# Performance work log

Hardware: AMD Instinct MI355X
Metric: run time of the kernel (lower is better)

Reference implementation:

```python
import jax, jax.numpy as jnp
import numpy as np

ATTEN = 32  # window half-size; window = 2*ATTEN + 1


def _pos_enc(seq_len, hidden_size):
    # Faithful to original: pos_enc[pos, j] = pos / 10000**(2*(j//2)/hidden_size)
    # then sin on even columns, cos on odd columns. Shape [seq_len, seq_len].
    pos = jnp.arange(seq_len, dtype=jnp.float32)[:, None]
    j = jnp.arange(seq_len)
    inv = jnp.power(jnp.float32(10000.0), (2.0 * (j // 2).astype(jnp.float32)) / hidden_size)
    angle = pos / inv[None, :]
    return jnp.where((j % 2 == 0)[None, :], jnp.sin(angle), jnp.cos(angle))


def setup_inputs() -> dict:
    key = jax.random.key(0)
    ks = jax.random.split(key, 8)
    B, S, D_in, H, D_out = 4, 2048, 2048, 128, 2
    sd_in = 1.0 / np.sqrt(D_in)
    sd_h = 1.0 / np.sqrt(H)
    return {
        "x": jax.random.normal(ks[0], (B, S, D_in), dtype=jnp.float32),
        "W1": jax.random.normal(ks[1], (D_in, H), dtype=jnp.float32) * sd_in,
        "b1": jnp.zeros((H,), dtype=jnp.float32),
        "Wq": jax.random.normal(ks[2], (H, H), dtype=jnp.float32) * sd_h,
        "Wk": jax.random.normal(ks[3], (H, H), dtype=jnp.float32) * sd_h,
        "Wv": jax.random.normal(ks[4], (H, H), dtype=jnp.float32) * sd_h,
        "Wo": jax.random.normal(ks[5], (H, D_out), dtype=jnp.float32) * sd_h,
        "bo": jnp.zeros((D_out,), dtype=jnp.float32),
    }


def reference(x, W1, b1, Wq, Wk, Wv, Wo, bo):
    B, S, _ = x.shape
    H = W1.shape[1]
    scale = jnp.float32(np.sqrt(float(H)))

    x = x + _pos_enc(S, H)[None]                      # [B,S,D_in] (D_in == S)
    h = jax.nn.relu(x @ W1 + b1)                      # [B,S,H]

    # Replicate pad + roll(+wraparound) + stack + slice via a gather.
    # x_nei[b,i,j] = padded[b, (i + 2a - j) mod (S+2a)], j in [0, 2a].
    a = ATTEN
    L = S + 2 * a
    padded = jnp.pad(h, ((0, 0), (a, a), (0, 0)))     # [B,L,H]
    idx = (jnp.arange(S)[:, None] + 2 * a - jnp.arange(2 * a + 1)[None, :]) % L
    x_nei = padded[:, idx, :]                         # [B,S,2a+1,H]

    q = h @ Wq                                        # [B,S,H]
    k = x_nei @ Wk                                    # [B,S,2a+1,H]
    v = x_nei @ Wv                                    # [B,S,2a+1,H]

    scores = jnp.einsum('bid,bijd->bij', q, k) / scale
    atten_weights = jax.nn.softmax(scores, axis=-1)   # [B,S,2a+1]
    context = jnp.einsum('bij,bijd->bid', atten_weights, v) / scale  # extra /sqrt(H), faithful to source
    output = context @ Wo + bo                        # [B,S,D_out]
    return output, atten_weights
```

## Files before the change

kernel.cpp:

```cpp
#include <hip/hip_runtime.h>
#include <hip/hip_bf16.h>

typedef __attribute__((ext_vector_type(8))) _Float16 half8;
typedef __attribute__((ext_vector_type(4))) _Float16 half4;
typedef __attribute__((ext_vector_type(4))) float f32x4;

#define MFMAH(a,b,c) __builtin_amdgcn_mfma_f32_16x16x32_f16(a,b,c,0,0,0)

__device__ __forceinline__ float posenc(float sf, int k) {
  float c = exp2f((float)(k >> 1) * -0.2076205059304595f) * 0.15915494309189535f;
  float p = sf * c;
  float r = __builtin_fmaf(sf, c, -rintf(p));
  return (k & 1) ? __builtin_amdgcn_cosf(r) : __builtin_amdgcn_sinf(r);
}

__global__ __launch_bounds__(256) void k_prep(const float* __restrict__ W1,
                                              const float* __restrict__ Wq,
                                              const float* __restrict__ Wk,
                                              const float* __restrict__ Wv,
                                              _Float16* __restrict__ W1t,
                                              _Float16* __restrict__ Wqkvt) {
  const int bid = blockIdx.x, tid = threadIdx.x;
  if (bid < 64) {
    __shared__ float Tl[64][65];
    const int kt0 = (bid >> 1) * 64, nt0 = (bid & 1) * 64;
    const int row = tid >> 2, c0 = (tid & 3) * 16;
#pragma unroll
    for (int e = 0; e < 16; e += 4) {
      float4 f = *(const float4*)(W1 + (size_t)(kt0 + row) * 128 + nt0 + c0 + e);
      Tl[row][c0 + e] = f.x; Tl[row][c0 + e + 1] = f.y;
      Tl[row][c0 + e + 2] = f.z; Tl[row][c0 + e + 3] = f.w;
    }
    __syncthreads();
    const int nrow = tid >> 2, kc0 = (tid & 3) * 16;
    _Float16* wp = W1t + (size_t)(nt0 + nrow) * 2048 + kt0 + kc0;
#pragma unroll
    for (int e = 0; e < 16; ++e) wp[e] = (_Float16)Tl[kc0 + e][nrow];
  } else {
    int r = (bid - 64) * 256 + tid;
    if (r < 3 * 16384) {
      int m = r >> 14, e = r & 16383;
      int n = e >> 7, k = e & 127;
      const float* W = (m == 0) ? Wq : (m == 1) ? Wk : Wv;
      Wqkvt[r] = (_Float16)W[k * 128 + n];
    }
  }
}

__global__ __launch_bounds__(512) void k_gemm1(const float* __restrict__ x,
                                               const _Float16* __restrict__ W1t,
                                               const float* __restrict__ b1,
                                               _Float16* __restrict__ hbuf) {
  __shared__ __align__(16) char smem[41472];
  const int tid = threadIdx.x;
  const int g = tid >> 8;
  const int gtid = tid & 255;
  const int lane = tid & 63;
  const int wv = (tid >> 6) & 3;
  _Float16 (*Al)[72] = (_Float16(*)[72])(smem + g * 2304);
  _Float16 (*Bl)[72] = (_Float16(*)[72])(smem + 4608 + g * 18432);
  const int i0 = blockIdx.x * 16;
  const int arow = gtid >> 4, akc = (gtid & 15) * 4;
  const int brow = gtid >> 1, bk0 = (gtid & 1) * 32;
  const int grow = i0 + arow;
  const float sf = (float)(grow & 2047);
  const int fr = lane & 15, kg = (lane >> 4) * 8;
  f32x4 acc[2] = {};
  for (int it = 0; it < 16; ++it) {
    const int kt = g * 1024 + it * 64;
    {
      float4 f = *(const float4*)(x + (size_t)grow * 2048 + kt + akc);
      half4 av;
      av[0] = (_Float16)(f.x + posenc(sf, kt + akc));
      av[1] = (_Float16)(f.y + posenc(sf, kt + akc + 1));
      av[2] = (_Float16)(f.z + posenc(sf, kt + akc + 2));
      av[3] = (_Float16)(f.w + posenc(sf, kt + akc + 3));
      *(half4*)&Al[arow][akc] = av;
    }
    {
      const _Float16* wp = W1t + (size_t)brow * 2048 + kt + bk0;
#pragma unroll
      for (int e = 0; e < 4; ++e)
        *(half8*)&Bl[brow][bk0 + e * 8] = *(const half8*)(wp + e * 8);
    }
    __syncthreads();
#pragma unroll
    for (int kk = 0; kk < 2; ++kk) {
      half8 a   = *(const half8*)&Al[fr][kk * 32 + kg];
      half8 b0  = *(const half8*)&Bl[wv * 32 + fr][kk * 32 + kg];
      half8 b1v = *(const half8*)&Bl[wv * 32 + 16 + fr][kk * 32 + kg];
      acc[0] = MFMAH(a, b0,  acc[0]);
      acc[1] = MFMAH(a, b1v, acc[1]);
    }
    __syncthreads();
  }
  float (*Cred)[128] = (float(*)[128])smem;
  if (g == 1) {
#pragma unroll
    for (int n2 = 0; n2 < 2; ++n2)
#pragma unroll
      for (int r = 0; r < 4; ++r)
        Cred[(lane >> 4) * 4 + r][wv * 32 + n2 * 16 + fr] = acc[n2][r];
  }
  __syncthreads();
  if (g == 0) {
#pragma unroll
    for (int n2 = 0; n2 < 2; ++n2) {
      const int col = wv * 32 + n2 * 16 + fr;
      const float bv = b1[col];
#pragma unroll
      for (int r = 0; r < 4; ++r) {
        const int row_l = (lane >> 4) * 4 + r;
        float v = acc[n2][r] + Cred[row_l][col] + bv;
        v = v > 0.f ? v : 0.f;
        hbuf[(size_t)(i0 + row_l) * 128 + col] = (_Float16)v;
      }
    }
  }
}

__global__ __launch_bounds__(256) void k_qkv(const _Float16* __restrict__ hbuf,
                                             const _Float16* __restrict__ Wtb,
                                             _Float16* __restrict__ outb) {
  __shared__ _Float16 Al[16][136];
  __shared__ _Float16 Bl[128][136];
  const int tid = threadIdx.x;
  const int lane = tid & 63, wv = tid >> 6;
  const int i0 = blockIdx.x * 16;
  const _Float16* Wt = Wtb + (size_t)blockIdx.y * 16384;
  _Float16* out = outb + (size_t)blockIdx.y * 1048576;
  {
    const int row = tid >> 4, c = (tid & 15) * 8;
    *(half8*)&Al[row][c] = *(const half8*)(hbuf + (size_t)(i0 + row) * 128 + c);
  }
  {
    const int n = tid >> 1, h0 = (tid & 1) * 64;
    const _Float16* wp = Wt + (size_t)n * 128 + h0;
#pragma unroll
    for (int e = 0; e < 8; ++e)
      *(half8*)&Bl[n][h0 + e * 8] = *(const half8*)(wp + e * 8);
  }
  __syncthreads();
  const int fr = lane & 15, kg = (lane >> 4) * 8;
  f32x4 acc[2] = {};
#pragma unroll
  for (int kk = 0; kk < 4; ++kk) {
    half8 a   = *(const half8*)&Al[fr][kk * 32 + kg];
    half8 b0  = *(const half8*)&Bl[wv * 32 + fr][kk * 32 + kg];
    half8 b1v = *(const half8*)&Bl[wv * 32 + 16 + fr][kk * 32 + kg];
    acc[0] = MFMAH(a, b0,  acc[0]);
    acc[1] = MFMAH(a, b1v, acc[1]);
  }
#pragma unroll
  for (int n2 = 0; n2 < 2; ++n2)
#pragma unroll
    for (int r = 0; r < 4; ++r) {
      const int row = i0 + (lane >> 4) * 4 + r;
      const int col = wv * 32 + n2 * 16 + fr;
      out[(size_t)row * 128 + col] = (_Float16)acc[n2][r];
    }
}

__global__ __launch_bounds__(256) void k_attn(const _Float16* __restrict__ Qg,
                                              const _Float16* __restrict__ Kg,
                                              const _Float16* __restrict__ Vg,
                                              const float* __restrict__ Wo,
                                              const float* __restrict__ bo,
                                              float* __restrict__ outp,
                                              float* __restrict__ attwg) {
  __shared__ _Float16 Qs[16][136];
  __shared__ _Float16 Ks[80][136];
  __shared__ _Float16 Vs[96][136];
  __shared__ _Float16 Ps[16][104];
  __shared__ float sc[16][84];
  __shared__ float aw[16 * 65];
  __shared__ float wol[128][2];
  __shared__ float proj[4][16][2];
  const int tid = threadIdx.x;
  const int lane = tid & 63, wv = tid >> 6;
  const int b = blockIdx.x >> 7;
  const int i0 = (blockIdx.x & 127) << 4;
  const int rowbase = b * 2048 + i0;
  const float invscale = 0.08838834764831845f;

  {
    const int row = tid >> 4, d8 = (tid & 15) * 8;
    *(half8*)&Qs[row][d8] = *(const half8*)(Qg + (size_t)(rowbase + row) * 128 + d8);
  }
#pragma unroll
  for (int it = 0; it < 5; ++it) {
    const int idx = it * 256 + tid;
    const int lr = idx >> 4, d8 = (idx & 15) * 8;
    const int j = i0 - 32 + lr;
    half8 kv = {0, 0, 0, 0, 0, 0, 0, 0};
    if (j >= 0 && j < 2048)
      kv = *(const half8*)(Kg + (size_t)(b * 2048 + j) * 128 + d8);
    *(half8*)&Ks[lr][d8] = kv;
  }
#pragma unroll
  for (int it = 0; it < 6; ++it) {
    const int idx = it * 256 + tid;
    const int lr = idx >> 4, d8 = (idx & 15) * 8;
    const int j = i0 - 32 + lr;
    half8 vv = {0, 0, 0, 0, 0, 0, 0, 0};
    if (lr < 80 && j >= 0 && j < 2048)
      vv = *(const half8*)(Vg + (size_t)(b * 2048 + j) * 128 + d8);
    *(half8*)&Vs[lr][d8] = vv;
  }
  wol[tid >> 1][tid & 1] = Wo[tid];
  __syncthreads();

  const int fr = lane & 15, kg8 = (lane >> 4) * 8;
  {
    const int nct = (wv == 0) ? 2 : 1;
    for (int p = 0; p < nct; ++p) {
      const int ct = (p == 0) ? wv : 4;
      f32x4 acc = {};
#pragma unroll
      for (int kk = 0; kk < 4; ++kk) {
        half8 a  = *(const half8*)&Qs[fr][kk * 32 + kg8];
        half8 bb = *(const half8*)&Ks[ct * 16 + fr][kk * 32 + kg8];
        acc = MFMAH(a, bb, acc);
      }
#pragma unroll
      for (int r = 0; r < 4; ++r)
        sc[(lane >> 4) * 4 + r][ct * 16 + fr] = acc[r] * invscale;
    }
  }
  __syncthreads();

#pragma unroll 1
  for (int rr = 0; rr < 4; ++rr) {
    const int r = wv * 4 + rr;
    const int c0 = lane;
    const bool ib0 = (c0 >= r);
    const bool ib1 = (lane <= r);
    float a0 = ib0 ? sc[r][c0] : -1e30f;
    float a1 = ib1 ? sc[r][64 + lane] : -1e30f;
    float mx = fmaxf(a0, a1);
#pragma unroll
    for (int o = 1; o < 64; o <<= 1) mx = fmaxf(mx, __shfl_xor(mx, o));
    float e0 = ib0 ? __expf(a0 - mx) : 0.f;
    float e1 = ib1 ? __expf(a1 - mx) : 0.f;
    float sm = e0 + e1;
#pragma unroll
    for (int o = 1; o < 64; o <<= 1) sm += __shfl_xor(sm, o);
    const float inv = 1.0f / sm;
    const float w0 = e0 * inv, w1 = e1 * inv;
    if (ib0) aw[r * 65 + (r + 64 - c0)] = w0;
    if (ib1) aw[r * 65 + (r - lane)] = w1;
    Ps[r][c0] = (_Float16)w0;
    if (lane < 32) Ps[r][64 + lane] = (_Float16)((lane < 16) ? w1 : 0.f);
  }
  __syncthreads();

  for (int i = tid; i < 1040; i += 256)
    attwg[(size_t)rowbase * 65 + i] = aw[i];

  f32x4 c2[2] = {};
#pragma unroll
  for (int kk = 0; kk < 3; ++kk) {
    half8 a = *(const half8*)&Ps[fr][kk * 32 + kg8];
#pragma unroll
    for (int dt2 = 0; dt2 < 2; ++dt2) {
      const int d = (2 * wv + dt2) * 16 + fr;
      half8 bb;
#pragma unroll
      for (int e = 0; e < 8; ++e) bb[e] = Vs[kk * 32 + kg8 + e][d];
      c2[dt2] = MFMAH(a, bb, c2[dt2]);
    }
  }
#pragma unroll
  for (int r = 0; r < 4; ++r) {
    float p0 = 0.f, p1 = 0.f;
#pragma unroll
    for (int dt2 = 0; dt2 < 2; ++dt2) {
      const int d = (2 * wv + dt2) * 16 + fr;
      p0 += c2[dt2][r] * wol[d][0];
      p1 += c2[dt2][r] * wol[d][1];
    }
    p0 += __shfl_xor(p0, 1); p0 += __shfl_xor(p0, 2);
    p0 += __shfl_xor(p0, 4); p0 += __shfl_xor(p0, 8);
    p1 += __shfl_xor(p1, 1); p1 += __shfl_xor(p1, 2);
    p1 += __shfl_xor(p1, 4); p1 += __shfl_xor(p1, 8);
    if (fr == 0) {
      const int q = (lane >> 4) * 4 + r;
      proj[wv][q][0] = p0;
      proj[wv][q][1] = p1;
    }
  }
  __syncthreads();
  if (tid < 16) {
    float s0 = proj[0][tid][0] + proj[1][tid][0] + proj[2][tid][0] + proj[3][tid][0];
    float s1 = proj[0][tid][1] + proj[1][tid][1] + proj[2][tid][1] + proj[3][tid][1];
    outp[((size_t)rowbase + tid) * 2 + 0] = s0 * invscale + bo[0];
    outp[((size_t)rowbase + tid) * 2 + 1] = s1 * invscale + bo[1];
  }
}

extern "C" void kernel_launch(void* const* d_in, const int* in_sizes, int n_in,
                              void* d_out, int out_size, void* d_ws, size_t ws_size,
                              hipStream_t stream) {
  const float* x  = (const float*)d_in[0];
  const float* W1 = (const float*)d_in[1];
  const float* b1 = (const float*)d_in[2];
  const float* Wq = (const float*)d_in[3];
  const float* Wk = (const float*)d_in[4];
  const float* Wv = (const float*)d_in[5];
  const float* Wo = (const float*)d_in[6];
  const float* bo = (const float*)d_in[7];
  float* out  = (float*)d_out;
  float* attw = out + 16384;

  _Float16* W1t  = (_Float16*)d_ws;
  _Float16* Wqkv = W1t + 262144;
  _Float16* hbuf = Wqkv + 49152;
  _Float16* Qg   = hbuf + 1048576;
  _Float16* Kg   = Qg + 1048576;
  _Float16* Vg   = Kg + 1048576;

  k_prep<<<256, 256, 0, stream>>>(W1, Wq, Wk, Wv, W1t, Wqkv);
  k_gemm1<<<512, 512, 0, stream>>>(x, W1t, b1, hbuf);
  k_qkv<<<dim3(512, 3), 256, 0, stream>>>(hbuf, Wqkv, Qg);
  k_attn<<<512, 256, 0, stream>>>(Qg, Kg, Vg, Wo, bo, out, attw);
}
```

Baseline: 49.97 us.

## Fuse W1 GEMM with QKV projection and double-buffer the K loop

Merges the input GEMM (with positional encoding, bias and ReLU) and the Q/K/V projections into one kernel. The hidden activations now stay in shared memory instead of going through a global buffer, and one launch is removed. The K loop drops the two-group split-K reduction in favour of a double-buffered register-prefetch pipeline over 128-wide K tiles across 8 waves. Each sin/cos pair now shares one frequency computation. The cost is higher shared-memory use per block, about 78 KB, which may limit occupancy, and the QKV phase runs serially inside each block.

After: 65.07 us. 1.3x slower.

```diff
diff --git a/kernel.cpp b/kernel.cpp
--- a/kernel.cpp
+++ b/kernel.cpp
@@ -7,12 +7,8 @@
 
 #define MFMAH(a,b,c) __builtin_amdgcn_mfma_f32_16x16x32_f16(a,b,c,0,0,0)
 
-__device__ __forceinline__ float posenc(float sf, int k) {
-  float c = exp2f((float)(k >> 1) * -0.2076205059304595f) * 0.15915494309189535f;
-  float p = sf * c;
-  float r = __builtin_fmaf(sf, c, -rintf(p));
-  return (k & 1) ? __builtin_amdgcn_cosf(r) : __builtin_amdgcn_sinf(r);
-}
+#define LOG2_10K_64 0.2076205059304595f
+#define INV2PI 0.15915494309189535f
 
 __global__ __launch_bounds__(256) void k_prep(const float* __restrict__ W1,
                                               const float* __restrict__ Wq,
@@ -47,118 +43,111 @@
   }
 }
 
-__global__ __launch_bounds__(512) void k_gemm1(const float* __restrict__ x,
+__global__ __launch_bounds__(512) void k_fused(const float* __restrict__ x,
                                                const _Float16* __restrict__ W1t,
+                                               const _Float16* __restrict__ Wqkv,
                                                const float* __restrict__ b1,
-                                               _Float16* __restrict__ hbuf) {
-  __shared__ __align__(16) char smem[41472];
-  const int tid = threadIdx.x;
-  const int g = tid >> 8;
-  const int gtid = tid & 255;
-  const int lane = tid & 63;
-  const int wv = (tid >> 6) & 3;
-  _Float16 (*Al)[72] = (_Float16(*)[72])(smem + g * 2304);
-  _Float16 (*Bl)[72] = (_Float16(*)[72])(smem + 4608 + g * 18432);
-  const int i0 = blockIdx.x * 16;
-  const int arow = gtid >> 4, akc = (gtid & 15) * 4;
-  const int brow = gtid >> 1, bk0 = (gtid & 1) * 32;
-  const int grow = i0 + arow;
-  const float sf = (float)(grow & 2047);
-  const int fr = lane & 15, kg = (lane >> 4) * 8;
-  f32x4 acc[2] = {};
-  for (int it = 0; it < 16; ++it) {
-    const int kt = g * 1024 + it * 64;
-    {
-      float4 f = *(const float4*)(x + (size_t)grow * 2048 + kt + akc);
-      half4 av;
-      av[0] = (_Float16)(f.x + posenc(sf, kt + akc));
-      av[1] = (_Float16)(f.y + posenc(sf, kt + akc + 1));
-      av[2] = (_Float16)(f.z + posenc(sf, kt + akc + 2));
-      av[3] = (_Float16)(f.w + posenc(sf, kt + akc + 3));
-      *(half4*)&Al[arow][akc] = av;
-    }
-    {
-      const _Float16* wp = W1t + (size_t)brow * 2048 + kt + bk0;
-#pragma unroll
-      for (int e = 0; e < 4; ++e)
-        *(half8*)&Bl[brow][bk0 + e * 8] = *(const half8*)(wp + e * 8);
-    }
-    __syncthreads();
-#pragma unroll
-    for (int kk = 0; kk < 2; ++kk) {
-      half8 a   = *(const half8*)&Al[fr][kk * 32 + kg];
-      half8 b0  = *(const half8*)&Bl[wv * 32 + fr][kk * 32 + kg];
-      half8 b1v = *(const half8*)&Bl[wv * 32 + 16 + fr][kk * 32 + kg];
-      acc[0] = MFMAH(a, b0,  acc[0]);
-      acc[1] = MFMAH(a, b1v, acc[1]);
-    }
-    __syncthreads();
-  }
-  float (*Cred)[128] = (float(*)[128])smem;
-  if (g == 1) {
-#pragma unroll
-    for (int n2 = 0; n2 < 2; ++n2)
-#pragma unroll
-      for (int r = 0; r < 4; ++r)
-        Cred[(lane >> 4) * 4 + r][wv * 32 + n2 * 16 + fr] = acc[n2][r];
-  }
-  __syncthreads();
-  if (g == 0) {
-#pragma unroll
-    for (int n2 = 0; n2 < 2; ++n2) {
-      const int col = wv * 32 + n2 * 16 + fr;
-      const float bv = b1[col];
-#pragma unroll
-      for (int r = 0; r < 4; ++r) {
-        const int row_l = (lane >> 4) * 4 + r;
-        float v = acc[n2][r] + Cred[row_l][col] + bv;
-        v = v > 0.f ? v : 0.f;
-        hbuf[(size_t)(i0 + row_l) * 128 + col] = (_Float16)v;
-      }
-    }
-  }
-}
-
-__global__ __launch_bounds__(256) void k_qkv(const _Float16* __restrict__ hbuf,
-                                             const _Float16* __restrict__ Wtb,
-                                             _Float16* __restrict__ outb) {
-  __shared__ _Float16 Al[16][136];
-  __shared__ _Float16 Bl[128][136];
+                                               _Float16* __restrict__ Qg,
+                                               _Float16* __restrict__ Kg,
+                                               _Float16* __restrict__ Vg) {
+  __shared__ __align__(16) char smem[78336];
   const int tid = threadIdx.x;
   const int lane = tid & 63, wv = tid >> 6;
   const int i0 = blockIdx.x * 16;
-  const _Float16* Wt = Wtb + (size_t)blockIdx.y * 16384;
-  _Float16* out = outb + (size_t)blockIdx.y * 1048576;
+  const int arow = tid >> 5, akc = (tid & 31) * 4;
+  const int brow = tid >> 2, bk = (tid & 3) * 32;
+  const float sf = (float)((i0 + arow) & 2047);
+  const int fr = lane & 15, kg8 = (lane >> 4) * 8;
+  const float* xrow = x + (size_t)(i0 + arow) * 2048;
+  const _Float16* wrow = W1t + (size_t)brow * 2048;
+
+  auto Albase = [&](int buf) { return (_Float16*)(smem + buf * 39168 + 34816); };
+  auto Blbase = [&](int buf) { return (_Float16*)(smem + buf * 39168); };
+
+  float4 xa;
+  half8 wb0, wb1, wb2, wb3;
+  auto issue_loads = [&](int kt) {
+    xa  = *(const float4*)(xrow + kt + akc);
+    wb0 = *(const half8*)(wrow + kt + bk);
+    wb1 = *(const half8*)(wrow + kt + bk + 8);
+    wb2 = *(const half8*)(wrow + kt + bk + 16);
+    wb3 = *(const half8*)(wrow + kt + bk + 24);
+  };
+  auto write_stage = [&](int buf, int kt) {
+    const int kb = kt + akc;
+    float c0 = exp2f((float)(kb >> 1) * -LOG2_10K_64) * INV2PI;
+    float c1 = exp2f((float)((kb >> 1) + 1) * -LOG2_10K_64) * INV2PI;
+    float r0 = __builtin_fmaf(sf, c0, -rintf(sf * c0));
+    float r1 = __builtin_fmaf(sf, c1, -rintf(sf * c1));
+    half4 av;
+    av[0] = (_Float16)(xa.x + __builtin_amdgcn_sinf(r0));
+    av[1] = (_Float16)(xa.y + __builtin_amdgcn_cosf(r0));
+    av[2] = (_Float16)(xa.z + __builtin_amdgcn_sinf(r1));
+    av[3] = (_Float16)(xa.w + __builtin_amdgcn_cosf(r1));
+    *(half4*)(Albase(buf) + arow * 136 + akc) = av;
+    _Float16* bl = Blbase(buf) + brow * 136 + bk;
+    *(half8*)(bl)      = wb0;
+    *(half8*)(bl + 8)  = wb1;
+    *(half8*)(bl + 16) = wb2;
+    *(half8*)(bl + 24) = wb3;
+  };
+
+  issue_loads(0);
+  write_stage(0, 0);
+  __syncthreads();
+
+  f32x4 acc = {};
+  for (int it = 0; it < 16; ++it) {
+    const int cur = it & 1;
+    const bool pf = (it < 15);
+    if (pf) issue_loads((it + 1) * 128);
+    const _Float16* Al = Albase(cur);
+    const _Float16* Bl = Blbase(cur) + (wv * 16 + fr) * 136;
+#pragma unroll
+    for (int kk = 0; kk < 4; ++kk) {
+      half8 a = *(const half8*)(Al + fr * 136 + kk * 32 + kg8);
+      half8 b = *(const half8*)(Bl + kk * 32 + kg8);
+      acc = MFMAH(a, b, acc);
+    }
+    if (pf) write_stage(cur ^ 1, (it + 1) * 128);
+    __syncthreads();
+  }
+
+  _Float16* Hs = Albase(0);
+  _Float16* Ws = Blbase(0);
   {
-    const int row = tid >> 4, c = (tid & 15) * 8;
-    *(half8*)&Al[row][c] = *(const half8*)(hbuf + (size_t)(i0 + row) * 128 + c);
-  }
-  {
-    const int n = tid >> 1, h0 = (tid & 1) * 64;
-    const _Float16* wp = Wt + (size_t)n * 128 + h0;
-#pragma unroll
-    for (int e = 0; e < 8; ++e)
-      *(half8*)&Bl[n][h0 + e * 8] = *(const half8*)(wp + e * 8);
-  }
-  __syncthreads();
-  const int fr = lane & 15, kg = (lane >> 4) * 8;
-  f32x4 acc[2] = {};
-#pragma unroll
-  for (int kk = 0; kk < 4; ++kk) {
-    half8 a   = *(const half8*)&Al[fr][kk * 32 + kg];
-    half8 b0  = *(const half8*)&Bl[wv * 32 + fr][kk * 32 + kg];
-    half8 b1v = *(const half8*)&Bl[wv * 32 + 16 + fr][kk * 32 + kg];
-    acc[0] = MFMAH(a, b0,  acc[0]);
-    acc[1] = MFMAH(a, b1v, acc[1]);
-  }
-#pragma unroll
-  for (int n2 = 0; n2 < 2; ++n2)
+    const int col = wv * 16 + fr;
+    const float bv = b1[col];
 #pragma unroll
     for (int r = 0; r < 4; ++r) {
-      const int row = i0 + (lane >> 4) * 4 + r;
-      const int col = wv * 32 + n2 * 16 + fr;
-      out[(size_t)row * 128 + col] = (_Float16)acc[n2][r];
-    }
+      float v = acc[r] + bv;
+      v = v > 0.f ? v : 0.f;
+      Hs[((lane >> 4) * 4 + r) * 136 + col] = (_Float16)v;
+    }
+  }
+  __syncthreads();
+#pragma unroll 1
+  for (int m = 0; m < 3; ++m) {
+    const _Float16* Wt = Wqkv + m * 16384 + (size_t)brow * 128;
+    _Float16* wl = Ws + brow * 136 + bk;
+    *(half8*)(wl)      = *(const half8*)(Wt + bk);
+    *(half8*)(wl + 8)  = *(const half8*)(Wt + bk + 8);
+    *(half8*)(wl + 16) = *(const half8*)(Wt + bk + 16);
+    *(half8*)(wl + 24) = *(const half8*)(Wt + bk + 24);
+    __syncthreads();
+    f32x4 a2 = {};
+#pragma unroll
+    for (int kk = 0; kk < 4; ++kk) {
+      half8 a = *(const half8*)(Hs + fr * 136 + kk * 32 + kg8);
+      half8 b = *(const half8*)(Ws + (wv * 16 + fr) * 136 + kk * 32 + kg8);
+      a2 = MFMAH(a, b, a2);
+    }
+    _Float16* dst = (m == 0) ? Qg : (m == 1) ? Kg : Vg;
+#pragma unroll
+    for (int r = 0; r < 4; ++r)
+      dst[(size_t)(i0 + (lane >> 4) * 4 + r) * 128 + wv * 16 + fr] = (_Float16)a2[r];
+    __syncthreads();
+  }
 }
 
 __global__ __launch_bounds__(256) void k_attn(const _Float16* __restrict__ Qg,
@@ -314,13 +303,11 @@
 
   _Float16* W1t  = (_Float16*)d_ws;
   _Float16* Wqkv = W1t + 262144;
-  _Float16* hbuf = Wqkv + 49152;
-  _Float16* Qg   = hbuf + 1048576;
+  _Float16* Qg   = Wqkv + 49152;
   _Float16* Kg   = Qg + 1048576;
   _Float16* Vg   = Kg + 1048576;
 
   k_prep<<<256, 256, 0, stream>>>(W1, Wq, Wk, Wv, W1t, Wqkv);
-  k_gemm1<<<512, 512, 0, stream>>>(x, W1t, b1, hbuf);
-  k_qkv<<<dim3(512, 3), 256, 0, stream>>>(hbuf, Wqkv, Qg);
+  k_fused<<<512, 512, 0, stream>>>(x, W1t, Wqkv, b1, Qg, Kg, Vg);
   k_attn<<<512, 256, 0, stream>>>(Qg, Kg, Vg, Wo, bo, out, attw);
 }
```
